# Optimization experiments

Measured on AMD Instinct MI355X. Metric: run time of the kernel, lower is better.

## Reference

```python
import jax, jax.numpy as jnp
import numpy as np

B, M, H, E = 1, 2048, 16, 128
D = H * E          # 2048, model dim
C = 4 * D          # 8192, FFN dim
F = E
G = D
J = D


def setup_inputs() -> dict:
    key = jax.random.key(0)
    k_in, k_wv, k_wk, k_wq, k_wz, k_ffa, k_ffb = jax.random.split(key, 7)
    scale = 0.01
    return {
        "I_in": jax.random.normal(k_in, (B, M, D), dtype=jnp.float32),
        "WV": jax.random.normal(k_wv, (H, E, D), dtype=jnp.float32) * scale,
        "WK": jax.random.normal(k_wk, (H, E, D), dtype=jnp.float32) * scale,
        "WQ": jax.random.normal(k_wq, (H, E, D), dtype=jnp.float32) * scale,
        "WZ": jax.random.normal(k_wz, (H, F, G), dtype=jnp.float32) * scale,
        "WFFA": jax.random.normal(k_ffa, (G, C), dtype=jnp.float32) * scale,
        "WFFB": jax.random.normal(k_ffb, (C, J), dtype=jnp.float32) * scale,
    }


def reference(I_in, WV, WK, WQ, WZ, WFFA, WFFB):
    # QKV projections: [B,M,D] x [H,E,D] -> [B,M,H,E]
    V = jnp.einsum('bmd,hed->bmhe', I_in, WV)
    K = jnp.einsum('bmd,hed->bmhe', I_in, WK)
    Q = jnp.einsum('bmd,hed->bmhe', I_in, WQ)
    # Attention scores [B,M,P,H]; NOTE: no 1/sqrt(E) scaling in the original.
    QK = jnp.einsum('bmhe,bphe->bmph', Q, K)
    # Softmax over keys (p axis = 2), matching torch.softmax(QK, dim=2)
    QK_softmax = jax.nn.softmax(QK, axis=2)
    # Attention output [B,M,H,E]
    AV = jnp.einsum('bmph,bphe->bmhe', QK_softmax, V)
    # Output projection [B,M,G]
    Z = jnp.einsum('bmhf,hfg->bmg', AV, WZ)
    # FFN (no nonlinearity in the original workload)
    FFA = jnp.einsum('bmg,gc->bmc', Z, WFFA)
    FFB = jnp.einsum('bmc,cj->bmj', FFA, WFFB)
    return FFB
```

## Files before the change

### kernel.cpp

```cpp
#include <hip/hip_runtime.h>
#include <hip/hip_bf16.h>
#include <math.h>


typedef __bf16 bf16_t;
typedef __bf16 bf16x8 __attribute__((ext_vector_type(8)));
typedef float  f32x4  __attribute__((ext_vector_type(4)));

#define AS1 __attribute__((address_space(1)))
#define AS3 __attribute__((address_space(3)))

__device__ __forceinline__ void load16_lds(const bf16_t* g, bf16_t* l) {
    __builtin_amdgcn_global_load_lds((AS1 void*)g, (AS3 void*)l, 16, 0, 0);
}

__device__ __forceinline__ float rowmax16(float v) {
    int t;
    t = __builtin_amdgcn_mov_dpp(__float_as_int(v), 0x128, 0xf, 0xf, true);
    v = fmaxf(v, __int_as_float(t));
    t = __builtin_amdgcn_mov_dpp(__float_as_int(v), 0x124, 0xf, 0xf, true);
    v = fmaxf(v, __int_as_float(t));
    t = __builtin_amdgcn_mov_dpp(__float_as_int(v), 0x122, 0xf, 0xf, true);
    v = fmaxf(v, __int_as_float(t));
    t = __builtin_amdgcn_mov_dpp(__float_as_int(v), 0x121, 0xf, 0xf, true);
    v = fmaxf(v, __int_as_float(t));
    return v;
}
__device__ __forceinline__ float rowsum16(float v) {
    int t;
    t = __builtin_amdgcn_mov_dpp(__float_as_int(v), 0x128, 0xf, 0xf, true);
    v += __int_as_float(t);
    t = __builtin_amdgcn_mov_dpp(__float_as_int(v), 0x124, 0xf, 0xf, true);
    v += __int_as_float(t);
    t = __builtin_amdgcn_mov_dpp(__float_as_int(v), 0x122, 0xf, 0xf, true);
    v += __int_as_float(t);
    t = __builtin_amdgcn_mov_dpp(__float_as_int(v), 0x121, 0xf, 0xf, true);
    v += __int_as_float(t);
    return v;
}

__device__ __forceinline__ void stageA_half(const bf16_t* __restrict__ Ab, int lda,
                                            int k0, int h, bf16_t* slot,
                                            int w, int lane)
{
    #pragma unroll
    for (int j = 0; j < 2; ++j) {
        const int prw = j * 64 + w * 8;
        const int p   = prw + (lane >> 3);
        const int lr  = (p >> 6) * 128 + h * 64 + (p & 63);
        const int lc  = (lane & 7) ^ (p & 7);
        load16_lds(Ab + (long long)lr * lda + k0 + lc * 8, slot + prw * 64);
    }
}
__device__ __forceinline__ void stageB_half(const bf16_t* __restrict__ Bb, int ldb,
                                            int k0, int h, bf16_t* slot,
                                            int w, int lane)
{
    #pragma unroll
    for (int j = 0; j < 2; ++j) {
        const int prw = j * 64 + w * 8;
        const int p   = prw + (lane >> 3);
        const int lr  = (p >> 5) * 64 + h * 32 + (p & 31);
        const int lc  = (lane & 7) ^ (p & 7);
        load16_lds(Bb + (long long)lr * ldb + k0 + lc * 8, slot + prw * 64);
    }
}

#define LOADAF(DST, SL)                                                        \
  _Pragma("unroll") for (int ks = 0; ks < 2; ++ks)                             \
  _Pragma("unroll") for (int mi = 0; mi < 4; ++mi)                             \
      DST[ks][mi] = *(const bf16x8*)&(SL)[(wm * 64 + mi * 16 + c15) * 64 +     \
                      (((ks * 4 + q4) ^ (c15 & 7)) * 8)];

#define LOADBV(DST, SL)                                                        \
  _Pragma("unroll") for (int ks = 0; ks < 2; ++ks)                             \
  _Pragma("unroll") for (int nj = 0; nj < 2; ++nj)                             \
      DST[ks][nj] = *(const bf16x8*)&(SL)[(wn * 32 + nj * 16 + c15) * 64 +     \
                      (((ks * 4 + q4) ^ (c15 & 7)) * 8)];

#define MFMA8(R0, C0)                                                          \
  _Pragma("unroll") for (int ks = 0; ks < 2; ++ks)                             \
  _Pragma("unroll") for (int mi = 0; mi < 4; ++mi)                             \
  _Pragma("unroll") for (int nj = 0; nj < 2; ++nj)                             \
      acc[(R0) + mi][(C0) + nj] = __builtin_amdgcn_mfma_f32_16x16x32_bf16(     \
          af[ks][mi], bv[ks][nj], acc[(R0) + mi][(C0) + nj], 0, 0, 0);

#define VMW(N)  asm volatile("s_waitcnt vmcnt(" #N ")" ::: "memory")
#define LGKM0() asm volatile("s_waitcnt lgkmcnt(0)" ::: "memory")
#define BAR()   __builtin_amdgcn_s_barrier()

#define PHASE8(RDS, STGS, GATE, R0, C0)                                        \
  RDS;                                                                         \
  STGS;                                                                        \
  GATE;                                                                        \
  __builtin_amdgcn_s_barrier();                                                \
  asm volatile("s_waitcnt lgkmcnt(0)" ::: "memory");                           \
  __builtin_amdgcn_sched_barrier(0);                                           \
  __builtin_amdgcn_s_setprio(1);                                               \
  MFMA8(R0, C0);                                                               \
  __builtin_amdgcn_s_setprio(0);                                               \
  __builtin_amdgcn_s_barrier();

template<typename TOUT>
__global__ __launch_bounds__(512, 2)
void gemm256p_bt(const bf16_t* __restrict__ A, const bf16_t* __restrict__ B,
                 TOUT* __restrict__ Cc, int Kdim,
                 int lda, int ldb, int ldc,
                 long long ab, long long bb, long long cb,
                 int ct_z, bf16_t* __restrict__ ctc, int ldct)
{
    __shared__ __attribute__((aligned(16))) bf16_t As4[4][128 * 64];
    __shared__ __attribute__((aligned(16))) bf16_t Bs4[4][128 * 64];

    const int z = blockIdx.z;
    A  += (long long)z * ab;
    B  += (long long)z * bb;
    Cc += (long long)z * cb;

    const int bm = blockIdx.y * 256;
    const int bn = blockIdx.x * 256;
    const int t = threadIdx.x, lane = t & 63, w = t >> 6;
    const int wm = w >> 2, wn = w & 3;
    const int q4 = lane >> 4, c15 = lane & 15;

    const bf16_t* Ab = A + (long long)bm * lda;
    const bf16_t* Bb = B + (long long)bn * ldb;

    f32x4  acc[8][4] = {};
    bf16x8 af[2][4];
    bf16x8 bv[2][2];

    stageB_half(Bb, ldb, 0,  0, Bs4[0], w, lane);
    stageA_half(Ab, lda, 0,  1, As4[1], w, lane);
    stageA_half(Ab, lda, 0,  0, As4[0], w, lane);
    stageB_half(Bb, ldb, 0,  1, Bs4[1], w, lane);
    stageB_half(Bb, ldb, 64, 0, Bs4[2], w, lane);
    stageA_half(Ab, lda, 64, 1, As4[3], w, lane);
    VMW(4);
    BAR();

    const int NT = Kdim >> 6;
    const int kcap = (NT - 1) << 6;

    for (int i = 0; i < NT / 2; ++i) {
        const int u  = 2 * i;
        const int k1 = (u + 1) << 6;
        int k2 = (u + 2) << 6; if (k2 > kcap) k2 = kcap;
        int k3 = (u + 3) << 6; if (k3 > kcap) k3 = kcap;
        PHASE8( LOADAF(af, As4[0]); LOADBV(bv, Bs4[0]),
                stageA_half(Ab, lda, k1, 0, As4[2], w, lane), ((void)0), 0, 0)
        PHASE8( LOADAF(af, As4[1]),
                stageB_half(Bb, ldb, k1, 1, Bs4[3], w, lane), ((void)0), 4, 0)
        PHASE8( LOADBV(bv, Bs4[1]),
                stageB_half(Bb, ldb, k2, 0, Bs4[0], w, lane), ((void)0), 4, 2)
        PHASE8( LOADAF(af, As4[0]),
                stageA_half(Ab, lda, k2, 1, As4[1], w, lane), VMW(4), 0, 2)
        PHASE8( LOADAF(af, As4[2]); LOADBV(bv, Bs4[2]),
                stageA_half(Ab, lda, k2, 0, As4[0], w, lane), ((void)0), 0, 0)
        PHASE8( LOADAF(af, As4[3]),
                stageB_half(Bb, ldb, k2, 1, Bs4[1], w, lane), ((void)0), 4, 0)
        PHASE8( LOADBV(bv, Bs4[3]),
                stageB_half(Bb, ldb, k3, 0, Bs4[2], w, lane), ((void)0), 4, 2)
        PHASE8( LOADAF(af, As4[2]),
                stageA_half(Ab, lda, k3, 1, As4[3], w, lane), VMW(4), 0, 2)
    }
    VMW(0);

    const int rb = q4 * 4;
    if (z == ct_z) {
        #pragma unroll
        for (int mi = 0; mi < 8; ++mi) {
            const long long mb = bm + wm * 128 + mi * 16 + rb;
            #pragma unroll
            for (int nj = 0; nj < 4; ++nj) {
                const long long n = bn + wn * 64 + nj * 16 + c15;
                union { bf16_t b[4]; unsigned long long u; } o;
                #pragma unroll
                for (int r = 0; r < 4; ++r) o.b[r] = (bf16_t)acc[mi][nj][r];
                *(unsigned long long*)(ctc + n * ldct + mb) = o.u;
            }
        }
    } else {
        #pragma unroll
        for (int mi = 0; mi < 8; ++mi) {
            #pragma unroll
            for (int r = 0; r < 4; ++r) {
                const long long m = bm + wm * 128 + mi * 16 + rb + r;
                TOUT* crow = Cc + m * ldc + bn + wn * 64 + c15;
                #pragma unroll
                for (int nj = 0; nj < 4; ++nj)
                    crow[nj * 16] = (TOUT)acc[mi][nj][r];
            }
        }
    }
}

__global__ __launch_bounds__(256, 2)
void flash_attn(const bf16_t* __restrict__ Q, const bf16_t* __restrict__ K,
                const bf16_t* __restrict__ VT, bf16_t* __restrict__ O,
                int M, int D)
{
    __shared__ bf16_t Kt[2][64 * 128];
    __shared__ bf16_t Vt[2][128 * 64];
    __shared__ bf16_t Pl[4 * 16 * 88];

    const int t = threadIdx.x, lane = t & 63, w = t >> 6;
    const int q4 = lane >> 4;
    const int c  = lane & 15;
    const int bm = blockIdx.x * 64;
    const int hE = blockIdx.y * 128;

    bf16x8 af_q[4];
    {
        const bf16_t* qrow = Q + (long long)(bm + w * 16 + c) * D + hE + q4 * 8;
        #pragma unroll
        for (int ks = 0; ks < 4; ++ks)
            af_q[ks] = *(const bf16x8*)(qrow + ks * 32);
    }

    f32x4 acc_o[8] = {};
    float m_i[4] = {-INFINITY, -INFINITY, -INFINITY, -INFINITY};
    float l_i[4] = {0.f, 0.f, 0.f, 0.f};

    bf16_t* Pw = &Pl[w * 16 * 88];

    const int NT = M >> 6;

    #define FA_STAGE(P0, B)                                                    \
      _Pragma("unroll")                                                        \
      for (int j = 0; j < 4; ++j) {                                            \
          int krow = w * 16 + j * 4;                                           \
          load16_lds(K + (long long)((P0) + krow + q4) * D + hE +              \
                         ((c ^ (j * 4 + q4)) * 8),                             \
                     &Kt[B][krow * 128]);                                      \
          int vrow = w * 32 + j * 8;                                           \
          load16_lds(VT + (long long)(hE + vrow + (lane >> 3)) * M + (P0) +    \
                         (((lane & 7) ^ (lane >> 3)) * 8),                     \
                     &Vt[B][vrow * 64]);                                       \
      }

    FA_STAGE(0, 0)

    for (int ti = 0; ti < NT; ++ti) {
        const int cur = ti & 1;
        const int pn = (ti + 1 < NT) ? (ti + 1) * 64 : ti * 64;
        FA_STAGE(pn, cur ^ 1)
        VMW(8);
        BAR();

        f32x4 acc_s[4] = {};
        __builtin_amdgcn_s_setprio(1);
        #pragma unroll
        for (int ks = 0; ks < 4; ++ks) {
            #pragma unroll
            for (int nj = 0; nj < 4; ++nj) {
                int row = nj * 16 + c;
                bf16x8 bk = *(const bf16x8*)&Kt[cur][row * 128 + (((ks * 4 + q4) ^ c) * 8)];
                acc_s[nj] = __builtin_amdgcn_mfma_f32_16x16x32_bf16(
                    af_q[ks], bk, acc_s[nj], 0, 0, 0);
            }
        }
        __builtin_amdgcn_s_setprio(0);

        float mt[4], rs[4];
        #pragma unroll
        for (int r = 0; r < 4; ++r) {
            mt[r] = rowmax16(fmaxf(fmaxf(acc_s[0][r], acc_s[1][r]),
                                   fmaxf(acc_s[2][r], acc_s[3][r])));
            rs[r] = 0.f;
        }
        bool ok = true;
        #pragma unroll
        for (int r = 0; r < 4; ++r) ok = ok && (mt[r] <= m_i[r] + 8.0f);
        if (__all(ok)) {
            #pragma unroll
            for (int nj = 0; nj < 4; ++nj)
                #pragma unroll
                for (int r = 0; r < 4; ++r) {
                    float p = __expf(acc_s[nj][r] - m_i[r]);
                    rs[r] += p;
                    Pw[(q4 * 4 + r) * 88 + nj * 16 + c] = (bf16_t)p;
                }
            #pragma unroll
            for (int r = 0; r < 4; ++r)
                l_i[r] += rowsum16(rs[r]);
        } else {
            float alpha[4];
            #pragma unroll
            for (int r = 0; r < 4; ++r) {
                float mn = fmaxf(m_i[r], mt[r]);
                alpha[r] = __expf(m_i[r] - mn);
                m_i[r] = mn;
            }
            #pragma unroll
            for (int nj = 0; nj < 4; ++nj)
                #pragma unroll
                for (int r = 0; r < 4; ++r) {
                    float p = __expf(acc_s[nj][r] - m_i[r]);
                    rs[r] += p;
                    Pw[(q4 * 4 + r) * 88 + nj * 16 + c] = (bf16_t)p;
                }
            #pragma unroll
            for (int r = 0; r < 4; ++r)
                l_i[r] = alpha[r] * l_i[r] + rowsum16(rs[r]);
            #pragma unroll
            for (int nj = 0; nj < 8; ++nj)
                #pragma unroll
                for (int r = 0; r < 4; ++r)
                    acc_o[nj][r] *= alpha[r];
        }

        LGKM0();
        __builtin_amdgcn_sched_barrier(0);

        __builtin_amdgcn_s_setprio(1);
        #pragma unroll
        for (int ks = 0; ks < 2; ++ks) {
            bf16x8 ap = *(const bf16x8*)&Pw[c * 88 + ks * 32 + q4 * 8];
            #pragma unroll
            for (int nj = 0; nj < 8; ++nj) {
                int row = nj * 16 + c;
                bf16x8 bvv = *(const bf16x8*)&Vt[cur][row * 64 + (((ks * 4 + q4) ^ (c & 7)) * 8)];
                acc_o[nj] = __builtin_amdgcn_mfma_f32_16x16x32_bf16(
                    ap, bvv, acc_o[nj], 0, 0, 0);
            }
        }
        __builtin_amdgcn_s_setprio(0);
        BAR();
    }
    VMW(0);

    float inv[4];
    #pragma unroll
    for (int r = 0; r < 4; ++r) inv[r] = 1.0f / l_i[r];
    #pragma unroll
    for (int nj = 0; nj < 8; ++nj)
        #pragma unroll
        for (int r = 0; r < 4; ++r)
            O[(long long)(bm + w * 16 + q4 * 4 + r) * D + hE + nj * 16 + c] =
                (bf16_t)(acc_o[nj][r] * inv[r]);
    #undef FA_STAGE
}

__global__ __launch_bounds__(256)
void cast4_bf16(const float* __restrict__ s0, const float* __restrict__ s1,
                const float* __restrict__ s2, const float* __restrict__ s3,
                bf16_t* __restrict__ d0, long long seg, long long n)
{
    const float* src = (blockIdx.y == 0) ? s0 : (blockIdx.y == 1) ? s1
                     : (blockIdx.y == 2) ? s2 : s3;
    bf16_t* dst = d0 + (long long)blockIdx.y * seg;
    long long i = ((long long)blockIdx.x * 256 + threadIdx.x) * 4;
    if (i >= n) return;
    float4 v = *(const float4*)(src + i);
    union { bf16_t b[4]; unsigned long long u; } o;
    o.b[0] = (bf16_t)v.x; o.b[1] = (bf16_t)v.y;
    o.b[2] = (bf16_t)v.z; o.b[3] = (bf16_t)v.w;
    *(unsigned long long*)(dst + i) = o.u;
}

__global__ __launch_bounds__(256)
void transpose_to_bf16(const float* __restrict__ in, bf16_t* __restrict__ out,
                       int rows, int cols)
{
    __shared__ bf16_t tile[32][33];
    const int r0 = blockIdx.y * 32, c0 = blockIdx.x * 32;
    const int tx = threadIdx.x & 31, ty = threadIdx.x >> 5;
    #pragma unroll
    for (int i = 0; i < 4; ++i) {
        int r = ty + i * 8;
        tile[r][tx] = (bf16_t)in[(long long)(r0 + r) * cols + c0 + tx];
    }
    __syncthreads();
    #pragma unroll
    for (int i = 0; i < 4; ++i) {
        int r = ty + i * 8;
        out[(long long)(c0 + r) * rows + r0 + tx] = tile[tx][r];
    }
}

__global__ __launch_bounds__(256)
void reduce4_f32(const float* __restrict__ p, float* __restrict__ out,
                 long long n)
{
    long long i = ((long long)blockIdx.x * 256 + threadIdx.x) * 4;
    if (i >= n) return;
    float4 a = *(const float4*)(p + i);
    float4 b = *(const float4*)(p + n + i);
    float4 c = *(const float4*)(p + 2 * n + i);
    float4 d = *(const float4*)(p + 3 * n + i);
    float4 o;
    o.x = a.x + b.x + c.x + d.x;
    o.y = a.y + b.y + c.y + d.y;
    o.z = a.z + b.z + c.z + d.z;
    o.w = a.w + b.w + c.w + d.w;
    *(float4*)(out + i) = o;
}

__global__ __launch_bounds__(256)
void reduce2_bf16(const float* __restrict__ p, bf16_t* __restrict__ out,
                  long long n)
{
    long long i = ((long long)blockIdx.x * 256 + threadIdx.x) * 4;
    if (i >= n) return;
    float4 a = *(const float4*)(p + i);
    float4 b = *(const float4*)(p + n + i);
    union { bf16_t b[4]; unsigned long long u; } o;
    o.b[0] = (bf16_t)(a.x + b.x);
    o.b[1] = (bf16_t)(a.y + b.y);
    o.b[2] = (bf16_t)(a.z + b.z);
    o.b[3] = (bf16_t)(a.w + b.w);
    *(unsigned long long*)(out + i) = o.u;
}

extern "C" void kernel_launch(void* const* d_in, const int* in_sizes, int n_in,
                              void* d_out, int out_size, void* d_ws, size_t ws_size,
                              hipStream_t stream)
{
    const float* I    = (const float*)d_in[0];
    const float* WV   = (const float*)d_in[1];
    const float* WK   = (const float*)d_in[2];
    const float* WQ   = (const float*)d_in[3];
    const float* WZ   = (const float*)d_in[4];
    const float* WFFA = (const float*)d_in[5];
    const float* WFFB = (const float*)d_in[6];
    float* out = (float*)d_out;

    const int M = 2048, D = 2048, C = 8192;
    const long long MD = (long long)M * D;
    const size_t MiB = 1024 * 1024;

    char* base = (char*)d_ws;
    bf16_t* bI     = (bf16_t*)(base + 0 * MiB);
    bf16_t* bWQ    = (bf16_t*)(base + 8 * MiB);
    bf16_t* bWK    = (bf16_t*)(base + 16 * MiB);
    bf16_t* bWV    = (bf16_t*)(base + 24 * MiB);
    bf16_t* bQ     = (bf16_t*)(base + 32 * MiB);
    bf16_t* bK     = (bf16_t*)(base + 40 * MiB);
    bf16_t* bVT    = (bf16_t*)(base + 48 * MiB);
    bf16_t* bAV    = (bf16_t*)(base + 56 * MiB);
    bf16_t* bZ     = (bf16_t*)(base + 64 * MiB);
    bf16_t* bWZT   = (bf16_t*)(base + 72 * MiB);
    bf16_t* bWFFAT = (bf16_t*)(base + 80 * MiB);
    bf16_t* bWFFBT = (bf16_t*)(base + 112 * MiB);
    bf16_t* bFFA   = (bf16_t*)(base + 0 * MiB);
    float*  pZ     = (float*)(base + 0 * MiB);
    float*  pF     = (float*)(base + 32 * MiB);

    const dim3 blk(256);
    const dim3 blk512(512);

    cast4_bf16<<<dim3(MD / 1024, 4), blk, 0, stream>>>(I, WQ, WK, WV, bI, MD, MD);
    transpose_to_bf16<<<dim3(D / 32, D / 32), blk, 0, stream>>>(WZ,   bWZT,   D, D);
    transpose_to_bf16<<<dim3(C / 32, D / 32), blk, 0, stream>>>(WFFA, bWFFAT, D, C);
    transpose_to_bf16<<<dim3(D / 32, C / 32), blk, 0, stream>>>(WFFB, bWFFBT, C, D);

    gemm256p_bt<bf16_t><<<dim3(8, 8, 3), blk512, 0, stream>>>(
        bI, bWQ, bQ, D, D, D, D, 0, MD, MD, 2, bVT, M);

    flash_attn<<<dim3(M / 64, 16), blk, 0, stream>>>(bQ, bK, bVT, bAV, M, D);

    gemm256p_bt<float><<<dim3(8, 8, 2), blk512, 0, stream>>>(
        bAV, bWZT, pZ, 1024, D, D, D, 1024, 1024, MD, -1, nullptr, 0);
    reduce2_bf16<<<dim3((int)(MD / 1024)), blk, 0, stream>>>(pZ, bZ, MD);

    gemm256p_bt<bf16_t><<<dim3(32, 8, 1), blk512, 0, stream>>>(
        bZ, bWFFAT, bFFA, D, D, D, C, 0, 0, 0, -1, nullptr, 0);

    gemm256p_bt<float><<<dim3(8, 8, 4), blk512, 0, stream>>>(
        bFFA, bWFFBT, pF, 2048, C, C, D, 2048, 2048, MD, -1, nullptr, 0);

    reduce4_f32<<<dim3((int)(MD / 1024)), blk, 0, stream>>>(pF, out, MD);
}
```

Baseline: 579.2 us.

## Swizzle workgroups across XCDs and double-buffer B fragments to cut LDS reads

Remaps the flat workgroup index so consecutive tiles land on the same XCD (8-way chiplet swizzle) in both the GEMM and flash-attention kernels, aiming to improve L2 reuse of shared A/B and K/V tiles. The GEMM inner loop now keeps two B-fragment register sets (bv0/bv1) and reorders the MFMA phases, so two phases reuse already-loaded fragments instead of re-reading A from LDS. This adds register pressure, and the swizzle assumes the workgroup count divides evenly by 8.

```diff
diff --git a/kernel.cpp b/kernel.cpp
--- a/kernel.cpp
+++ b/kernel.cpp
@@ -78,18 +78,18 @@
       DST[ks][nj] = *(const bf16x8*)&(SL)[(wn * 32 + nj * 16 + c15) * 64 +     \
                       (((ks * 4 + q4) ^ (c15 & 7)) * 8)];
 
-#define MFMA8(R0, C0)                                                          \
+#define MFMA8(R0, C0, BV)                                                      \
   _Pragma("unroll") for (int ks = 0; ks < 2; ++ks)                             \
   _Pragma("unroll") for (int mi = 0; mi < 4; ++mi)                             \
   _Pragma("unroll") for (int nj = 0; nj < 2; ++nj)                             \
       acc[(R0) + mi][(C0) + nj] = __builtin_amdgcn_mfma_f32_16x16x32_bf16(     \
-          af[ks][mi], bv[ks][nj], acc[(R0) + mi][(C0) + nj], 0, 0, 0);
+          af[ks][mi], BV[ks][nj], acc[(R0) + mi][(C0) + nj], 0, 0, 0);
 
 #define VMW(N)  asm volatile("s_waitcnt vmcnt(" #N ")" ::: "memory")
 #define LGKM0() asm volatile("s_waitcnt lgkmcnt(0)" ::: "memory")
 #define BAR()   __builtin_amdgcn_s_barrier()
 
-#define PHASE8(RDS, STGS, GATE, R0, C0)                                        \
+#define PHASE8(RDS, STGS, GATE, R0, C0, BV)                                    \
   RDS;                                                                         \
   STGS;                                                                        \
   GATE;                                                                        \
@@ -97,7 +97,7 @@
   asm volatile("s_waitcnt lgkmcnt(0)" ::: "memory");                           \
   __builtin_amdgcn_sched_barrier(0);                                           \
   __builtin_amdgcn_s_setprio(1);                                               \
-  MFMA8(R0, C0);                                                               \
+  MFMA8(R0, C0, BV);                                                           \
   __builtin_amdgcn_s_setprio(0);                                               \
   __builtin_amdgcn_s_barrier();
 
@@ -112,13 +112,22 @@
     __shared__ __attribute__((aligned(16))) bf16_t As4[4][128 * 64];
     __shared__ __attribute__((aligned(16))) bf16_t Bs4[4][128 * 64];
 
-    const int z = blockIdx.z;
+    const int nx = gridDim.x, ny = gridDim.y;
+    const int nwg = nx * ny * gridDim.z;
+    const int flat = blockIdx.x + nx * (blockIdx.y + ny * blockIdx.z);
+    const int cpx = nwg >> 3;
+    const int swz = (flat & 7) * cpx + (flat >> 3);
+    const int bx = swz % nx;
+    const int tmp = swz / nx;
+    const int by = tmp % ny;
+    const int z  = tmp / ny;
+
     A  += (long long)z * ab;
     B  += (long long)z * bb;
     Cc += (long long)z * cb;
 
-    const int bm = blockIdx.y * 256;
-    const int bn = blockIdx.x * 256;
+    const int bm = by * 256;
+    const int bn = bx * 256;
     const int t = threadIdx.x, lane = t & 63, w = t >> 6;
     const int wm = w >> 2, wn = w & 3;
     const int q4 = lane >> 4, c15 = lane & 15;
@@ -128,7 +137,8 @@
 
     f32x4  acc[8][4] = {};
     bf16x8 af[2][4];
-    bf16x8 bv[2][2];
+    bf16x8 bv0[2][2];
+    bf16x8 bv1[2][2];
 
     stageB_half(Bb, ldb, 0,  0, Bs4[0], w, lane);
     stageA_half(Ab, lda, 0,  1, As4[1], w, lane);
@@ -147,22 +157,22 @@
         const int k1 = (u + 1) << 6;
         int k2 = (u + 2) << 6; if (k2 > kcap) k2 = kcap;
         int k3 = (u + 3) << 6; if (k3 > kcap) k3 = kcap;
-        PHASE8( LOADAF(af, As4[0]); LOADBV(bv, Bs4[0]),
-                stageA_half(Ab, lda, k1, 0, As4[2], w, lane), ((void)0), 0, 0)
+        PHASE8( LOADAF(af, As4[0]); LOADBV(bv0, Bs4[0]),
+                stageA_half(Ab, lda, k1, 0, As4[2], w, lane), ((void)0), 0, 0, bv0)
+        PHASE8( LOADBV(bv1, Bs4[1]),
+                stageB_half(Bb, ldb, k1, 1, Bs4[3], w, lane), ((void)0), 0, 2, bv1)
         PHASE8( LOADAF(af, As4[1]),
-                stageB_half(Bb, ldb, k1, 1, Bs4[3], w, lane), ((void)0), 4, 0)
-        PHASE8( LOADBV(bv, Bs4[1]),
-                stageB_half(Bb, ldb, k2, 0, Bs4[0], w, lane), ((void)0), 4, 2)
-        PHASE8( LOADAF(af, As4[0]),
-                stageA_half(Ab, lda, k2, 1, As4[1], w, lane), VMW(4), 0, 2)
-        PHASE8( LOADAF(af, As4[2]); LOADBV(bv, Bs4[2]),
-                stageA_half(Ab, lda, k2, 0, As4[0], w, lane), ((void)0), 0, 0)
+                stageB_half(Bb, ldb, k2, 0, Bs4[0], w, lane), ((void)0), 4, 2, bv1)
+        PHASE8( ((void)0),
+                stageA_half(Ab, lda, k2, 1, As4[1], w, lane), VMW(4), 4, 0, bv0)
+        PHASE8( LOADAF(af, As4[2]); LOADBV(bv0, Bs4[2]),
+                stageA_half(Ab, lda, k2, 0, As4[0], w, lane), ((void)0), 0, 0, bv0)
+        PHASE8( LOADBV(bv1, Bs4[3]),
+                stageB_half(Bb, ldb, k2, 1, Bs4[1], w, lane), ((void)0), 0, 2, bv1)
         PHASE8( LOADAF(af, As4[3]),
-                stageB_half(Bb, ldb, k2, 1, Bs4[1], w, lane), ((void)0), 4, 0)
-        PHASE8( LOADBV(bv, Bs4[3]),
-                stageB_half(Bb, ldb, k3, 0, Bs4[2], w, lane), ((void)0), 4, 2)
-        PHASE8( LOADAF(af, As4[2]),
-                stageA_half(Ab, lda, k3, 1, As4[3], w, lane), VMW(4), 0, 2)
+                stageB_half(Bb, ldb, k3, 0, Bs4[2], w, lane), ((void)0), 4, 2, bv1)
+        PHASE8( ((void)0),
+                stageA_half(Ab, lda, k3, 1, As4[3], w, lane), VMW(4), 4, 0, bv0)
     }
     VMW(0);
 
@@ -207,8 +217,13 @@
     const int t = threadIdx.x, lane = t & 63, w = t >> 6;
     const int q4 = lane >> 4;
     const int c  = lane & 15;
-    const int bm = blockIdx.x * 64;
-    const int hE = blockIdx.y * 128;
+
+    const int nwg = gridDim.x * gridDim.y;
+    const int flat = blockIdx.x + gridDim.x * blockIdx.y;
+    const int cpx = nwg >> 3;
+    const int swz = (flat & 7) * cpx + (flat >> 3);
+    const int bm = (swz % gridDim.x) * 64;
+    const int hE = (swz / gridDim.x) * 128;
 
     bf16x8 af_q[4];
     {
```

After: 564.4 us. 1.03x faster.
